# Optimization experiments

Measured on AMD Instinct MI355X. Metric: run time of the kernel, lower is better.

## Reference

```python
import jax, jax.numpy as jnp
import numpy as np

HIDDEN = 1024
HEADS = 16
B, L = 2, 2048


def _xavier(key, shape):
    fan_in, fan_out = shape[1], shape[0]
    limit = float(np.sqrt(6.0 / (fan_in + fan_out)))
    return jax.random.uniform(key, shape, jnp.float32, -limit, limit)


def setup_inputs() -> dict:
    key = jax.random.key(0)
    ks = jax.random.split(key, 6)
    return {
        "query": jax.random.normal(ks[0], (B, L, HIDDEN), jnp.float32),
        "bias": jax.random.normal(ks[1], (B, 1, 1, L), jnp.float32),
        "Wq": _xavier(ks[2], (HIDDEN, HIDDEN)), "bq": jnp.zeros((HIDDEN,), jnp.float32),
        "Wk": _xavier(ks[3], (HIDDEN, HIDDEN)), "bk": jnp.zeros((HIDDEN,), jnp.float32),
        "Wv": _xavier(ks[4], (HIDDEN, HIDDEN)), "bv": jnp.zeros((HIDDEN,), jnp.float32),
        "Wo": _xavier(ks[5], (HIDDEN, HIDDEN)), "bo": jnp.zeros((HIDDEN,), jnp.float32),
    }


def _split_heads(x):
    b, l, c = x.shape
    return x.reshape(b, l, HEADS, c // HEADS).transpose(0, 2, 1, 3)  # [B,H,L,d]


def reference(query, bias, Wq, bq, Wk, bk, Wv, bv, Wo, bo):
    d_head = HIDDEN // HEADS
    q = query @ Wq.T + bq
    k = query @ Wk.T + bk
    v = query @ Wv.T + bv
    q = _split_heads(q) * (d_head ** -0.5)  # [B,H,L,d]
    k = _split_heads(k)
    v = _split_heads(v)
    logits = jnp.einsum("bhqd,bhkd->bhqk", q, k) + bias  # [B,H,L,L]
    weights = jax.nn.softmax(logits, axis=-1)
    x = jnp.einsum("bhqk,bhkd->bhqd", weights, v)  # [B,H,L,d]
    x = x.transpose(0, 2, 1, 3).reshape(query.shape[0], query.shape[1], HIDDEN)
    return x @ Wo.T + bo
```

## Files before the change

### kernel.cpp

```cpp
#include <hip/hip_runtime.h>
#include <hip/hip_fp16.h>
#include <stdint.h>

#define HIDDEN 1024
#define HEADS  16
#define DH     64
#define B_     2
#define L_     2048
#define M_TOT  (B_ * L_)
#define ELEMS  (M_TOT * HIDDEN)
#define LOG2E  1.44269504088896340736f

typedef _Float16 f16;
typedef _Float16 f16x4 __attribute__((ext_vector_type(4)));
typedef _Float16 f16x8 __attribute__((ext_vector_type(8)));
typedef float    f32x4 __attribute__((ext_vector_type(4)));
typedef uint32_t u32;
typedef __attribute__((address_space(1))) u32 gu32;
typedef __attribute__((address_space(3))) u32 su32;

#define MFMA32(a, b, c) __builtin_amdgcn_mfma_f32_16x16x32_f16(a, b, c, 0, 0, 0)


__global__ __launch_bounds__(256)
void convert_f16(const float* __restrict__ query,
                 const float* __restrict__ Wq, const float* __restrict__ Wk,
                 const float* __restrict__ Wv, const float* __restrict__ Wo,
                 f16* __restrict__ Qh, f16* __restrict__ Wh)
{
    const int NQ4 = ELEMS / 4;
    const int NW4 = (HIDDEN * HIDDEN) / 4;
    const int total = NQ4 + 4 * NW4;
    for (int u = blockIdx.x * 256 + threadIdx.x; u < total; u += gridDim.x * 256) {
        float4 v; f16* dp;
        if (u < NQ4) {
            v = ((const float4*)query)[u];
            dp = Qh + (size_t)u * 4;
        } else {
            const int u2 = u - NQ4;
            const int w = u2 >> 18;
            const int off = u2 & (NW4 - 1);
            const float* W = (w == 0) ? Wq : (w == 1) ? Wk : (w == 2) ? Wv : Wo;
            v = ((const float4*)W)[off];
            dp = Wh + (size_t)u2 * 4;
        }
        f16x4 h = { (f16)v.x, (f16)v.y, (f16)v.z, (f16)v.w };
        *(f16x4*)dp = h;
    }
}

template<int TM, int TN, bool SWAP>
__device__ __forceinline__
void gemm_loop(const f16* __restrict__ A, const f16* __restrict__ W,
               int mb, int nb, f32x4 (&acc)[TM / 32][TN / 32])
{
    extern __shared__ f16 smem[];
    f16* As = smem;
    f16* Bs = smem + 3 * TM * 32;

    const int tid  = threadIdx.x;
    const int lane = tid & 63;
    const int wave = tid >> 6;
    const int quad = lane >> 4;
    const int l16  = lane & 15;
    const int wm   = (wave >> 1) * (TM / 2);
    const int wn   = (wave & 1) * (TN / 2);

    constexpr int AISS = TM / 64;
    constexpr int BISS = TN / 64;
    int aoff[AISS], boff[BISS];
#pragma unroll
    for (int q = 0; q < AISS; q++) {
        const int p16 = (wave * AISS + q) * 64 + lane;
        const int r = p16 >> 2;
        const int c8 = (p16 & 3) ^ ((r >> 1) & 3);
        aoff[q] = (mb + r) * HIDDEN + c8 * 8;
    }
#pragma unroll
    for (int q = 0; q < BISS; q++) {
        const int p16 = (wave * BISS + q) * 64 + lane;
        const int r = p16 >> 2;
        const int c8 = (p16 & 3) ^ ((r >> 1) & 3);
        boff[q] = (nb + r) * HIDDEN + c8 * 8;
    }

#pragma unroll
    for (int p = 0; p < 2; p++) {
#pragma unroll
        for (int q = 0; q < AISS; q++)
            __builtin_amdgcn_global_load_lds((gu32*)&A[aoff[q] + p * 32],
                                             (su32*)&As[p * TM * 32 + (wave * AISS + q) * 512], 16, 0, 0);
#pragma unroll
        for (int q = 0; q < BISS; q++)
            __builtin_amdgcn_global_load_lds((gu32*)&W[boff[q] + p * 32],
                                             (su32*)&Bs[p * TN * 32 + (wave * BISS + q) * 512], 16, 0, 0);
    }

    int sl = 0;
#pragma unroll 1
    for (int kb = 0; kb < HIDDEN; kb += 32) {
        if constexpr (AISS + BISS == 4)
            asm volatile("s_waitcnt vmcnt(4)" ::: "memory");
        else
            asm volatile("s_waitcnt vmcnt(3)" ::: "memory");
        __builtin_amdgcn_s_barrier();
        __builtin_amdgcn_sched_barrier(0);

        const int nkb = (kb + 64 < HIDDEN) ? kb + 64 : 0;
        const int si  = (sl >= 1) ? sl - 1 : 2;
#pragma unroll
        for (int q = 0; q < AISS; q++)
            __builtin_amdgcn_global_load_lds((gu32*)&A[aoff[q] + nkb],
                                             (su32*)&As[si * TM * 32 + (wave * AISS + q) * 512], 16, 0, 0);
#pragma unroll
        for (int q = 0; q < BISS; q++)
            __builtin_amdgcn_global_load_lds((gu32*)&W[boff[q] + nkb],
                                             (su32*)&Bs[si * TN * 32 + (wave * BISS + q) * 512], 16, 0, 0);

        f16x8 af[TM / 32], bf[TN / 32];
#pragma unroll
        for (int i = 0; i < TM / 32; i++) {
            const int r = wm + i * 16 + l16;
            af[i] = *(const f16x8*)&As[sl * TM * 32 + r * 32 + (quad ^ ((r >> 1) & 3)) * 8];
        }
#pragma unroll
        for (int j = 0; j < TN / 32; j++) {
            const int r = wn + j * 16 + l16;
            bf[j] = *(const f16x8*)&Bs[sl * TN * 32 + r * 32 + (quad ^ ((r >> 1) & 3)) * 8];
        }
#pragma unroll
        for (int i = 0; i < TM / 32; i++)
#pragma unroll
            for (int j = 0; j < TN / 32; j++) {
                if constexpr (SWAP)
                    acc[i][j] = MFMA32(bf[j], af[i], acc[i][j]);
                else
                    acc[i][j] = MFMA32(af[i], bf[j], acc[i][j]);
            }

        sl = (sl + 1 == 3) ? 0 : sl + 1;
    }
    asm volatile("s_waitcnt vmcnt(0)" ::: "memory");
}

__global__ __launch_bounds__(256)
void proj_qkv(const f16* __restrict__ A, const f16* __restrict__ W,
              const float* __restrict__ bq, const float* __restrict__ bk,
              const float* __restrict__ bv,
              f16* __restrict__ Qo, f16* __restrict__ Ko, f16* __restrict__ Vo)
{
    f32x4 acc[4][4] = {};
    const int mb = blockIdx.x * 128, nb = blockIdx.y * 128;
    const int nsel = nb >> 10;
    if (nsel < 2) gemm_loop<128, 128, true >(A, W, mb, nb, acc);
    else          gemm_loop<128, 128, false>(A, W, mb, nb, acc);

    const int lane = threadIdx.x & 63, wave = threadIdx.x >> 6;
    const int quad = lane >> 4, l16 = lane & 15;
    const int wm = (wave >> 1) * 64, wn = (wave & 1) * 64;
    const int nbase = nb & 1023;

    if (nsel < 2) {
        const float* bias = nsel ? bk : bq;
        f16* out = nsel ? Ko : Qo;
        const float scale = nsel ? 1.0f : 0.125f * LOG2E;
#pragma unroll
        for (int i = 0; i < 4; i++) {
            const int m = mb + wm + i * 16 + l16;
            const int b = m >> 11, l = m & (L_ - 1);
#pragma unroll
            for (int j = 0; j < 4; j++) {
                const int n0 = nbase + wn + j * 16 + quad * 4;
                const f32x4 bl4 = *(const f32x4*)&bias[n0];
                const int h = n0 >> 6, dd = n0 & 63;
                f16x4 pk;
#pragma unroll
                for (int r = 0; r < 4; r++)
                    pk[r] = (f16)((acc[i][j][r] + bl4[r]) * scale);
                *(f16x4*)&out[(((b * HEADS + h) * L_) + l) * DH + dd] = pk;
            }
        }
    } else {
#pragma unroll
        for (int i = 0; i < 4; i++)
#pragma unroll
            for (int j = 0; j < 4; j++) {
                const int n1 = nbase + wn + j * 16 + l16;
                const float bn = bv[n1];
                const int h = n1 >> 6, dd = n1 & 63;
                const int m0 = mb + wm + i * 16 + quad * 4;
                const int b = m0 >> 11, l0 = m0 & (L_ - 1);
                f16x4 pk;
#pragma unroll
                for (int r = 0; r < 4; r++) pk[r] = (f16)(acc[i][j][r] + bn);
                *(f16x4*)&Vo[((size_t)(b * HEADS + h) * DH + dd) * L_ + l0] = pk;
            }
    }
}

__global__ __launch_bounds__(256)
void proj_out(const f16* __restrict__ A, const f16* __restrict__ W,
              const float* __restrict__ bo, float* __restrict__ out)
{
    f32x4 acc[4][2] = {};
    const int mb = blockIdx.x * 128, nb = blockIdx.y * 64;
    gemm_loop<128, 64, true>(A, W, mb, nb, acc);

    const int lane = threadIdx.x & 63, wave = threadIdx.x >> 6;
    const int quad = lane >> 4, l16 = lane & 15;
    const int wm = (wave >> 1) * 64, wn = (wave & 1) * 32;
#pragma unroll
    for (int i = 0; i < 4; i++) {
        const int m = mb + wm + i * 16 + l16;
#pragma unroll
        for (int j = 0; j < 2; j++) {
            const int n0 = nb + wn + j * 16 + quad * 4;
            const float4 b4 = *(const float4*)&bo[n0];
            float4 st;
            st.x = acc[i][j][0] + b4.x;
            st.y = acc[i][j][1] + b4.y;
            st.z = acc[i][j][2] + b4.z;
            st.w = acc[i][j][3] + b4.w;
            *(float4*)&out[m * HIDDEN + n0] = st;
        }
    }
}

__global__ __launch_bounds__(512, 4)
void attn(const f16* __restrict__ Q, const f16* __restrict__ K,
          const f16* __restrict__ Vt, const float* __restrict__ bias,
          f16* __restrict__ X)
{
    __shared__ f16 Ks[2][2][64 * 64];
    __shared__ f16 Vs[2][2][64 * 64];
    __shared__ float biasl[L_];

    const int tid  = threadIdx.x;
    const int lane = tid & 63;
    const int wave = tid >> 6;
    const int quad = lane >> 4;
    const int l16  = lane & 15;
    const int qg   = wave >> 1;
    const int g    = wave & 1;

    const int bid = (int)blockIdx.x;
    const int lb  = (bid & 7) * 64 + (bid >> 3);
    const int bh  = lb >> 4;
    const int b   = bh >> 4, h = bh & 15;
    const int qrow0 = (lb & 15) * 128 + qg * 32;

    const f16* Qh  = Q  + (size_t)bh * L_ * DH;
    const f16* Kh  = K  + (size_t)bh * L_ * DH;
    const f16* Vth = Vt + (size_t)bh * DH * L_;

    {
        const float4 v = ((const float4*)(bias + b * L_))[tid];
        biasl[tid * 4 + 0] = v.x * LOG2E;
        biasl[tid * 4 + 1] = v.y * LOG2E;
        biasl[tid * 4 + 2] = v.z * LOG2E;
        biasl[tid * 4 + 3] = v.w * LOG2E;
    }

    int krow, kcol, vcol;
    {
        const int p = wave * 64 + lane;
        const int r = p >> 3;
        const int w8 = p & 7;
        krow = r;
        kcol = (w8 ^ (r & 7) ^ (((r >> 3) & 1) << 2)) * 8;
        vcol = (w8 ^ (r & 7)) * 8;
    }

    f16x8 qf[2][2];
#pragma unroll
    for (int qt = 0; qt < 2; qt++)
#pragma unroll
        for (int hh = 0; hh < 2; hh++)
            qf[qt][hh] = *(const f16x8*)&Qh[(qrow0 + qt * 16 + l16) * DH + hh * 32 + quad * 8];

    int koffX[2], koffY[2], voff[4];
    {
        const int rX = g * 32 + ((l16 >> 2) << 3) + (l16 & 3);
        const int rY = rX + 4;
        const int gkX = (rX & 7) ^ (((rX >> 3) & 1) << 2);
        const int gkY = (rY & 7) ^ (((rY >> 3) & 1) << 2);
#pragma unroll
        for (int hh = 0; hh < 2; hh++) {
            koffX[hh] = rX * 64 + (((hh * 4 + quad) ^ gkX) << 3);
            koffY[hh] = rY * 64 + (((hh * 4 + quad) ^ gkY) << 3);
        }
#pragma unroll
        for (int t = 0; t < 4; t++) {
            const int vr = t * 16 + l16;
            voff[t] = vr * 64 + (((g * 4 + quad) ^ (vr & 7)) << 3);
        }
    }

#pragma unroll
    for (int gi = 0; gi < 2; gi++) {
        __builtin_amdgcn_global_load_lds(
            (gu32*)(Kh + (size_t)(gi * 64 + krow) * DH + kcol),
            (su32*)&Ks[0][gi][wave * 512], 16, 0, 0);
        __builtin_amdgcn_global_load_lds(
            (gu32*)(Vth + (size_t)krow * L_ + gi * 64 + vcol),
            (su32*)&Vs[0][gi][wave * 512], 16, 0, 0);
    }

    f32x4 o[2][4] = {};
    f32x4 osum[2] = {};
    const f16x8 ones8 = { (f16)1.f, (f16)1.f, (f16)1.f, (f16)1.f,
                          (f16)1.f, (f16)1.f, (f16)1.f, (f16)1.f };
    __syncthreads();

#pragma unroll 1
    for (int kb = 0; kb < L_; kb += 128) {
        const int buf = (kb >> 7) & 1;
        const int nkb = (kb + 128 < L_) ? kb + 128 : 0;

#pragma unroll
        for (int gi = 0; gi < 2; gi++) {
            __builtin_amdgcn_global_load_lds(
                (gu32*)(Kh + (size_t)(nkb + gi * 64 + krow) * DH + kcol),
                (su32*)&Ks[buf ^ 1][gi][wave * 512], 16, 0, 0);
            __builtin_amdgcn_global_load_lds(
                (gu32*)(Vth + (size_t)krow * L_ + nkb + gi * 64 + vcol),
                (su32*)&Vs[buf ^ 1][gi][wave * 512], 16, 0, 0);
        }

#pragma unroll
        for (int gi = 0; gi < 2; gi++) {
            const f16* Kb = &Ks[buf][gi][0];
            const f16* Vb = &Vs[buf][gi][0];
            const f16x8 kx0 = *(const f16x8*)&Kb[koffX[0]];
            const f16x8 kx1 = *(const f16x8*)&Kb[koffX[1]];
            const f16x8 ky0 = *(const f16x8*)&Kb[koffY[0]];
            const f16x8 ky1 = *(const f16x8*)&Kb[koffY[1]];
            f16x8 va[4];
#pragma unroll
            for (int t = 0; t < 4; t++)
                va[t] = *(const f16x8*)&Vb[voff[t]];
            const f32x4 blvX = *(const f32x4*)&biasl[kb + gi * 64 + g * 32 + quad * 8];
            const f32x4 blvY = *(const f32x4*)&biasl[kb + gi * 64 + g * 32 + quad * 8 + 4];

#pragma unroll
            for (int qt = 0; qt < 2; qt++) {
                f32x4 zx = blvX, zy = blvY;
                zx = MFMA32(kx0, qf[qt][0], zx);
                zx = MFMA32(kx1, qf[qt][1], zx);
                zy = MFMA32(ky0, qf[qt][0], zy);
                zy = MFMA32(ky1, qf[qt][1], zy);
                const f16x8 pb = {
                    (f16)__builtin_amdgcn_exp2f(zx[0]), (f16)__builtin_amdgcn_exp2f(zx[1]),
                    (f16)__builtin_amdgcn_exp2f(zx[2]), (f16)__builtin_amdgcn_exp2f(zx[3]),
                    (f16)__builtin_amdgcn_exp2f(zy[0]), (f16)__builtin_amdgcn_exp2f(zy[1]),
                    (f16)__builtin_amdgcn_exp2f(zy[2]), (f16)__builtin_amdgcn_exp2f(zy[3]) };
#pragma unroll
                for (int t = 0; t < 4; t++)
                    o[qt][t] = MFMA32(va[t], pb, o[qt][t]);
                osum[qt] = MFMA32(ones8, pb, osum[qt]);
            }
        }
        __syncthreads();
    }

    float* o0 = (float*)Ks;
    float* o1 = (float*)Vs;
    if (g) {
#pragma unroll
        for (int t = 0; t < 4; t++)
#pragma unroll
            for (int r = 0; r < 4; r++) {
                o0[(qg * 16 + t * 4 + r) * 64 + lane] = o[0][t][r];
                o1[(qg * 16 + t * 4 + r) * 64 + lane] = o[1][t][r];
            }
        biasl[(qg * 64 + lane) * 2 + 0] = osum[0][0];
        biasl[(qg * 64 + lane) * 2 + 1] = osum[1][0];
    }
    __syncthreads();
    if (!g) {
#pragma unroll
        for (int t = 0; t < 4; t++)
#pragma unroll
            for (int r = 0; r < 4; r++) {
                o[0][t][r] += o0[(qg * 16 + t * 4 + r) * 64 + lane];
                o[1][t][r] += o1[(qg * 16 + t * 4 + r) * 64 + lane];
            }
        const float s0 = osum[0][0] + biasl[(qg * 64 + lane) * 2 + 0];
        const float s1 = osum[1][0] + biasl[(qg * 64 + lane) * 2 + 1];
#pragma unroll
        for (int qt = 0; qt < 2; qt++) {
            const float inv = 1.0f / (qt ? s1 : s0);
            const size_t qrow = (size_t)b * L_ + qrow0 + qt * 16 + l16;
#pragma unroll
            for (int t = 0; t < 4; t++) {
                f16x4 pk;
#pragma unroll
                for (int r = 0; r < 4; r++) pk[r] = (f16)(o[qt][t][r] * inv);
                *(f16x4*)&X[qrow * HIDDEN + h * DH + t * 16 + quad * 4] = pk;
            }
        }
    }
}

extern "C" void kernel_launch(void* const* d_in, const int* in_sizes, int n_in,
                              void* d_out, int out_size, void* d_ws, size_t ws_size,
                              hipStream_t stream)
{
    const float* query = (const float*)d_in[0];
    const float* bias  = (const float*)d_in[1];
    const float* Wq = (const float*)d_in[2]; const float* bq = (const float*)d_in[3];
    const float* Wk = (const float*)d_in[4]; const float* bk = (const float*)d_in[5];
    const float* Wv = (const float*)d_in[6]; const float* bv = (const float*)d_in[7];
    const float* Wo = (const float*)d_in[8]; const float* bo = (const float*)d_in[9];
    float* out = (float*)d_out;

    f16* Wh = (f16*)d_ws;
    f16* Qh = Wh + 4096 * 1024;
    f16* Kf = Qh + ELEMS;
    f16* Vf = Kf + ELEMS;
    f16* Qf = Vf + ELEMS;
    f16* Xf = Qh;

    convert_f16<<<2048, 256, 0, stream>>>(query, Wq, Wk, Wv, Wo, Qh, Wh);
    proj_qkv<<<dim3(32, 24), 256, 49152, stream>>>(Qh, Wh, bq, bk, bv, Qf, Kf, Vf);
    attn<<<512, 512, 0, stream>>>(Qf, Kf, Vf, bias, Xf);
    proj_out<<<dim3(32, 16), 256, 36864, stream>>>(Xf, Wh + 3072 * 1024, bo, out);
}
```

Before: 188.0 us.

## Split attention key chunks across twice as many waves with two-level reduction

The attention block grows from 512 to 1024 threads. Each wave now processes one 64-key sub-chunk per iteration instead of two, so four waves share each query group and each wave issues a single async K/V LDS load. Partial outputs and row sums are then combined in a two-stage LDS reduction. This raises wave-level parallelism and halves per-wave serial work, at the cost of extra barriers and reduction traffic, and it requires launch bounds of 1024 threads with 8 waves per EU.

```diff
diff --git a/kernel.cpp b/kernel.cpp
--- a/kernel.cpp
+++ b/kernel.cpp
@@ -226,7 +226,7 @@
     }
 }
 
-__global__ __launch_bounds__(512, 4)
+__global__ __launch_bounds__(1024, 8)
 void attn(const f16* __restrict__ Q, const f16* __restrict__ K,
           const f16* __restrict__ Vt, const float* __restrict__ bias,
           f16* __restrict__ X)
@@ -240,8 +240,12 @@
     const int wave = tid >> 6;
     const int quad = lane >> 4;
     const int l16  = lane & 15;
-    const int qg   = wave >> 1;
-    const int g    = wave & 1;
+    const int qg   = wave >> 2;
+    const int g4   = wave & 3;
+    const int cgi  = g4 >> 1;
+    const int g    = g4 & 1;
+    const int sgi  = wave >> 3;
+    const int sw   = wave & 7;
 
     const int bid = (int)blockIdx.x;
     const int lb  = (bid & 7) * 64 + (bid >> 3);
@@ -254,16 +258,14 @@
     const f16* Vth = Vt + (size_t)bh * DH * L_;
 
     {
-        const float4 v = ((const float4*)(bias + b * L_))[tid];
-        biasl[tid * 4 + 0] = v.x * LOG2E;
-        biasl[tid * 4 + 1] = v.y * LOG2E;
-        biasl[tid * 4 + 2] = v.z * LOG2E;
-        biasl[tid * 4 + 3] = v.w * LOG2E;
+        const float2 v2 = ((const float2*)(bias + b * L_))[tid];
+        biasl[tid * 2 + 0] = v2.x * LOG2E;
+        biasl[tid * 2 + 1] = v2.y * LOG2E;
     }
 
     int krow, kcol, vcol;
     {
-        const int p = wave * 64 + lane;
+        const int p = sw * 64 + lane;
         const int r = p >> 3;
         const int w8 = p & 7;
         krow = r;
@@ -296,15 +298,12 @@
         }
     }
 
-#pragma unroll
-    for (int gi = 0; gi < 2; gi++) {
-        __builtin_amdgcn_global_load_lds(
-            (gu32*)(Kh + (size_t)(gi * 64 + krow) * DH + kcol),
-            (su32*)&Ks[0][gi][wave * 512], 16, 0, 0);
-        __builtin_amdgcn_global_load_lds(
-            (gu32*)(Vth + (size_t)krow * L_ + gi * 64 + vcol),
-            (su32*)&Vs[0][gi][wave * 512], 16, 0, 0);
-    }
+    __builtin_amdgcn_global_load_lds(
+        (gu32*)(Kh + (size_t)(sgi * 64 + krow) * DH + kcol),
+        (su32*)&Ks[0][sgi][sw * 512], 16, 0, 0);
+    __builtin_amdgcn_global_load_lds(
+        (gu32*)(Vth + (size_t)krow * L_ + sgi * 64 + vcol),
+        (su32*)&Vs[0][sgi][sw * 512], 16, 0, 0);
 
     f32x4 o[2][4] = {};
     f32x4 osum[2] = {};
@@ -317,76 +316,97 @@
         const int buf = (kb >> 7) & 1;
         const int nkb = (kb + 128 < L_) ? kb + 128 : 0;
 
-#pragma unroll
-        for (int gi = 0; gi < 2; gi++) {
-            __builtin_amdgcn_global_load_lds(
-                (gu32*)(Kh + (size_t)(nkb + gi * 64 + krow) * DH + kcol),
-                (su32*)&Ks[buf ^ 1][gi][wave * 512], 16, 0, 0);
-            __builtin_amdgcn_global_load_lds(
-                (gu32*)(Vth + (size_t)krow * L_ + nkb + gi * 64 + vcol),
-                (su32*)&Vs[buf ^ 1][gi][wave * 512], 16, 0, 0);
-        }
-
-#pragma unroll
-        for (int gi = 0; gi < 2; gi++) {
-            const f16* Kb = &Ks[buf][gi][0];
-            const f16* Vb = &Vs[buf][gi][0];
-            const f16x8 kx0 = *(const f16x8*)&Kb[koffX[0]];
-            const f16x8 kx1 = *(const f16x8*)&Kb[koffX[1]];
-            const f16x8 ky0 = *(const f16x8*)&Kb[koffY[0]];
-            const f16x8 ky1 = *(const f16x8*)&Kb[koffY[1]];
-            f16x8 va[4];
+        __builtin_amdgcn_global_load_lds(
+            (gu32*)(Kh + (size_t)(nkb + sgi * 64 + krow) * DH + kcol),
+            (su32*)&Ks[buf ^ 1][sgi][sw * 512], 16, 0, 0);
+        __builtin_amdgcn_global_load_lds(
+            (gu32*)(Vth + (size_t)krow * L_ + nkb + sgi * 64 + vcol),
+            (su32*)&Vs[buf ^ 1][sgi][sw * 512], 16, 0, 0);
+
+        const f16* Kb = &Ks[buf][cgi][0];
+        const f16* Vb = &Vs[buf][cgi][0];
+        const f16x8 kx0 = *(const f16x8*)&Kb[koffX[0]];
+        const f16x8 kx1 = *(const f16x8*)&Kb[koffX[1]];
+        const f16x8 ky0 = *(const f16x8*)&Kb[koffY[0]];
+        const f16x8 ky1 = *(const f16x8*)&Kb[koffY[1]];
+        f16x8 va[4];
+#pragma unroll
+        for (int t = 0; t < 4; t++)
+            va[t] = *(const f16x8*)&Vb[voff[t]];
+        const f32x4 blvX = *(const f32x4*)&biasl[kb + cgi * 64 + g * 32 + quad * 8];
+        const f32x4 blvY = *(const f32x4*)&biasl[kb + cgi * 64 + g * 32 + quad * 8 + 4];
+
+#pragma unroll
+        for (int qt = 0; qt < 2; qt++) {
+            f32x4 zx = blvX, zy = blvY;
+            zx = MFMA32(kx0, qf[qt][0], zx);
+            zx = MFMA32(kx1, qf[qt][1], zx);
+            zy = MFMA32(ky0, qf[qt][0], zy);
+            zy = MFMA32(ky1, qf[qt][1], zy);
+            const f16x8 pb = {
+                (f16)__builtin_amdgcn_exp2f(zx[0]), (f16)__builtin_amdgcn_exp2f(zx[1]),
+                (f16)__builtin_amdgcn_exp2f(zx[2]), (f16)__builtin_amdgcn_exp2f(zx[3]),
+                (f16)__builtin_amdgcn_exp2f(zy[0]), (f16)__builtin_amdgcn_exp2f(zy[1]),
+                (f16)__builtin_amdgcn_exp2f(zy[2]), (f16)__builtin_amdgcn_exp2f(zy[3]) };
 #pragma unroll
             for (int t = 0; t < 4; t++)
-                va[t] = *(const f16x8*)&Vb[voff[t]];
-            const f32x4 blvX = *(const f32x4*)&biasl[kb + gi * 64 + g * 32 + quad * 8];
-            const f32x4 blvY = *(const f32x4*)&biasl[kb + gi * 64 + g * 32 + quad * 8 + 4];
-
-#pragma unroll
-            for (int qt = 0; qt < 2; qt++) {
-                f32x4 zx = blvX, zy = blvY;
-                zx = MFMA32(kx0, qf[qt][0], zx);
-                zx = MFMA32(kx1, qf[qt][1], zx);
-                zy = MFMA32(ky0, qf[qt][0], zy);
-                zy = MFMA32(ky1, qf[qt][1], zy);
-                const f16x8 pb = {
-                    (f16)__builtin_amdgcn_exp2f(zx[0]), (f16)__builtin_amdgcn_exp2f(zx[1]),
-                    (f16)__builtin_amdgcn_exp2f(zx[2]), (f16)__builtin_amdgcn_exp2f(zx[3]),
-                    (f16)__builtin_amdgcn_exp2f(zy[0]), (f16)__builtin_amdgcn_exp2f(zy[1]),
-                    (f16)__builtin_amdgcn_exp2f(zy[2]), (f16)__builtin_amdgcn_exp2f(zy[3]) };
-#pragma unroll
-                for (int t = 0; t < 4; t++)
-                    o[qt][t] = MFMA32(va[t], pb, o[qt][t]);
-                osum[qt] = MFMA32(ones8, pb, osum[qt]);
-            }
+                o[qt][t] = MFMA32(va[t], pb, o[qt][t]);
+            osum[qt] = MFMA32(ones8, pb, osum[qt]);
         }
         __syncthreads();
     }
 
-    float* o0 = (float*)Ks;
-    float* o1 = (float*)Vs;
-    if (g) {
+    float* r0 = (float*)Ks;
+    float* r1 = (float*)Vs;
+    float s0 = osum[0][0], s1 = osum[1][0];
+
+    const int s1slot = qg * 2 + cgi;
+    if (g4 & 1) {
 #pragma unroll
         for (int t = 0; t < 4; t++)
 #pragma unroll
             for (int r = 0; r < 4; r++) {
-                o0[(qg * 16 + t * 4 + r) * 64 + lane] = o[0][t][r];
-                o1[(qg * 16 + t * 4 + r) * 64 + lane] = o[1][t][r];
-            }
-        biasl[(qg * 64 + lane) * 2 + 0] = osum[0][0];
-        biasl[(qg * 64 + lane) * 2 + 1] = osum[1][0];
+                r0[s1slot * 1024 + (t * 4 + r) * 64 + lane] = o[0][t][r];
+                r1[s1slot * 1024 + (t * 4 + r) * 64 + lane] = o[1][t][r];
+            }
+        biasl[s1slot * 128 + lane * 2 + 0] = s0;
+        biasl[s1slot * 128 + lane * 2 + 1] = s1;
     }
     __syncthreads();
-    if (!g) {
+    if (!(g4 & 1)) {
 #pragma unroll
         for (int t = 0; t < 4; t++)
 #pragma unroll
             for (int r = 0; r < 4; r++) {
-                o[0][t][r] += o0[(qg * 16 + t * 4 + r) * 64 + lane];
-                o[1][t][r] += o1[(qg * 16 + t * 4 + r) * 64 + lane];
-            }
-        const float s0 = osum[0][0] + biasl[(qg * 64 + lane) * 2 + 0];
-        const float s1 = osum[1][0] + biasl[(qg * 64 + lane) * 2 + 1];
+                o[0][t][r] += r0[s1slot * 1024 + (t * 4 + r) * 64 + lane];
+                o[1][t][r] += r1[s1slot * 1024 + (t * 4 + r) * 64 + lane];
+            }
+        s0 += biasl[s1slot * 128 + lane * 2 + 0];
+        s1 += biasl[s1slot * 128 + lane * 2 + 1];
+    }
+    __syncthreads();
+    if (g4 == 2) {
+#pragma unroll
+        for (int t = 0; t < 4; t++)
+#pragma unroll
+            for (int r = 0; r < 4; r++) {
+                r0[qg * 1024 + (t * 4 + r) * 64 + lane] = o[0][t][r];
+                r1[qg * 1024 + (t * 4 + r) * 64 + lane] = o[1][t][r];
+            }
+        biasl[1024 + qg * 128 + lane * 2 + 0] = s0;
+        biasl[1024 + qg * 128 + lane * 2 + 1] = s1;
+    }
+    __syncthreads();
+    if (g4 == 0) {
+#pragma unroll
+        for (int t = 0; t < 4; t++)
+#pragma unroll
+            for (int r = 0; r < 4; r++) {
+                o[0][t][r] += r0[qg * 1024 + (t * 4 + r) * 64 + lane];
+                o[1][t][r] += r1[qg * 1024 + (t * 4 + r) * 64 + lane];
+            }
+        s0 += biasl[1024 + qg * 128 + lane * 2 + 0];
+        s1 += biasl[1024 + qg * 128 + lane * 2 + 1];
 #pragma unroll
         for (int qt = 0; qt < 2; qt++) {
             const float inv = 1.0f / (qt ? s1 : s0);
@@ -423,6 +443,6 @@
 
     convert_f16<<<2048, 256, 0, stream>>>(query, Wq, Wk, Wv, Wo, Qh, Wh);
     proj_qkv<<<dim3(32, 24), 256, 49152, stream>>>(Qh, Wh, bq, bk, bv, Qf, Kf, Vf);
-    attn<<<512, 512, 0, stream>>>(Qf, Kf, Vf, bias, Xf);
+    attn<<<512, 1024, 0, stream>>>(Qf, Kf, Vf, bias, Xf);
     proj_out<<<dim3(32, 16), 256, 36864, stream>>>(Xf, Wh + 3072 * 1024, bo, out);
 }
```

After: 553.9 us. 195% more time.

## Fuse fp32-to-fp16 conversion into projection GEMM loads, drop convert kernel

Applied to the files above, without the earlier changes.

Removes the separate conversion kernel and has the projection GEMMs read fp32 query and weights directly, converting to fp16 in registers before writing to LDS. The pipeline changes from a 3-stage async global_load_lds ring to a double-buffered register-staged scheme with __syncthreads each k-step. The intent is to save a kernel launch and the extra round trip of writing and re-reading fp16 copies. The cost is twice the global bytes per GEMM load, conversion ALU work inside the loop, and a shallower prefetch with heavier synchronisation.

```diff
diff --git a/kernel.cpp b/kernel.cpp
--- a/kernel.cpp
+++ b/kernel.cpp
@@ -22,41 +22,14 @@
 #define MFMA32(a, b, c) __builtin_amdgcn_mfma_f32_16x16x32_f16(a, b, c, 0, 0, 0)
 
 
-__global__ __launch_bounds__(256)
-void convert_f16(const float* __restrict__ query,
-                 const float* __restrict__ Wq, const float* __restrict__ Wk,
-                 const float* __restrict__ Wv, const float* __restrict__ Wo,
-                 f16* __restrict__ Qh, f16* __restrict__ Wh)
-{
-    const int NQ4 = ELEMS / 4;
-    const int NW4 = (HIDDEN * HIDDEN) / 4;
-    const int total = NQ4 + 4 * NW4;
-    for (int u = blockIdx.x * 256 + threadIdx.x; u < total; u += gridDim.x * 256) {
-        float4 v; f16* dp;
-        if (u < NQ4) {
-            v = ((const float4*)query)[u];
-            dp = Qh + (size_t)u * 4;
-        } else {
-            const int u2 = u - NQ4;
-            const int w = u2 >> 18;
-            const int off = u2 & (NW4 - 1);
-            const float* W = (w == 0) ? Wq : (w == 1) ? Wk : (w == 2) ? Wv : Wo;
-            v = ((const float4*)W)[off];
-            dp = Wh + (size_t)u2 * 4;
-        }
-        f16x4 h = { (f16)v.x, (f16)v.y, (f16)v.z, (f16)v.w };
-        *(f16x4*)dp = h;
-    }
-}
-
-template<int TM, int TN, bool SWAP>
+template<int TM, int TN, bool SWAP, bool A32, bool B32, typename TA, typename TB>
 __device__ __forceinline__
-void gemm_loop(const f16* __restrict__ A, const f16* __restrict__ W,
+void gemm_loop(const TA* __restrict__ A, const TB* __restrict__ W,
                int mb, int nb, f32x4 (&acc)[TM / 32][TN / 32])
 {
     extern __shared__ f16 smem[];
     f16* As = smem;
-    f16* Bs = smem + 3 * TM * 32;
+    f16* Bs = smem + 2 * TM * 32;
 
     const int tid  = threadIdx.x;
     const int lane = tid & 63;
@@ -68,13 +41,14 @@
 
     constexpr int AISS = TM / 64;
     constexpr int BISS = TN / 64;
-    int aoff[AISS], boff[BISS];
+    int aoff[AISS], boff[BISS], au[AISS], bu[BISS];
 #pragma unroll
     for (int q = 0; q < AISS; q++) {
         const int p16 = (wave * AISS + q) * 64 + lane;
         const int r = p16 >> 2;
         const int c8 = (p16 & 3) ^ ((r >> 1) & 3);
         aoff[q] = (mb + r) * HIDDEN + c8 * 8;
+        au[q] = p16;
     }
 #pragma unroll
     for (int q = 0; q < BISS; q++) {
@@ -82,51 +56,74 @@
         const int r = p16 >> 2;
         const int c8 = (p16 & 3) ^ ((r >> 1) & 3);
         boff[q] = (nb + r) * HIDDEN + c8 * 8;
-    }
-
-#pragma unroll
-    for (int p = 0; p < 2; p++) {
-#pragma unroll
-        for (int q = 0; q < AISS; q++)
-            __builtin_amdgcn_global_load_lds((gu32*)&A[aoff[q] + p * 32],
-                                             (su32*)&As[p * TM * 32 + (wave * AISS + q) * 512], 16, 0, 0);
-#pragma unroll
-        for (int q = 0; q < BISS; q++)
-            __builtin_amdgcn_global_load_lds((gu32*)&W[boff[q] + p * 32],
-                                             (su32*)&Bs[p * TN * 32 + (wave * BISS + q) * 512], 16, 0, 0);
-    }
-
-    int sl = 0;
+        bu[q] = p16;
+    }
+
+#pragma unroll
+    for (int q = 0; q < AISS; q++) {
+        if constexpr (A32) {
+            const float4 u0 = *(const float4*)&A[aoff[q]];
+            const float4 u1 = *(const float4*)&A[aoff[q] + 4];
+            f16x8 hv = { (f16)u0.x, (f16)u0.y, (f16)u0.z, (f16)u0.w,
+                         (f16)u1.x, (f16)u1.y, (f16)u1.z, (f16)u1.w };
+            *(f16x8*)&As[au[q] * 8] = hv;
+        } else {
+            __builtin_amdgcn_global_load_lds((gu32*)&A[aoff[q]],
+                                             (su32*)&As[(wave * AISS + q) * 512], 16, 0, 0);
+        }
+    }
+#pragma unroll
+    for (int q = 0; q < BISS; q++) {
+        if constexpr (B32) {
+            const float4 u0 = *(const float4*)&W[boff[q]];
+            const float4 u1 = *(const float4*)&W[boff[q] + 4];
+            f16x8 hv = { (f16)u0.x, (f16)u0.y, (f16)u0.z, (f16)u0.w,
+                         (f16)u1.x, (f16)u1.y, (f16)u1.z, (f16)u1.w };
+            *(f16x8*)&Bs[bu[q] * 8] = hv;
+        } else {
+            __builtin_amdgcn_global_load_lds((gu32*)&W[boff[q]],
+                                             (su32*)&Bs[(wave * BISS + q) * 512], 16, 0, 0);
+        }
+    }
+    __syncthreads();
+
 #pragma unroll 1
     for (int kb = 0; kb < HIDDEN; kb += 32) {
-        if constexpr (AISS + BISS == 4)
-            asm volatile("s_waitcnt vmcnt(4)" ::: "memory");
-        else
-            asm volatile("s_waitcnt vmcnt(3)" ::: "memory");
-        __builtin_amdgcn_s_barrier();
-        __builtin_amdgcn_sched_barrier(0);
-
-        const int nkb = (kb + 64 < HIDDEN) ? kb + 64 : 0;
-        const int si  = (sl >= 1) ? sl - 1 : 2;
-#pragma unroll
-        for (int q = 0; q < AISS; q++)
-            __builtin_amdgcn_global_load_lds((gu32*)&A[aoff[q] + nkb],
-                                             (su32*)&As[si * TM * 32 + (wave * AISS + q) * 512], 16, 0, 0);
-#pragma unroll
-        for (int q = 0; q < BISS; q++)
-            __builtin_amdgcn_global_load_lds((gu32*)&W[boff[q] + nkb],
-                                             (su32*)&Bs[si * TN * 32 + (wave * BISS + q) * 512], 16, 0, 0);
+        const int buf = (kb >> 5) & 1;
+        const int nkb = (kb + 32 < HIDDEN) ? kb + 32 : 0;
+
+        float4 fa0[AISS], fa1[AISS], fb0[BISS], fb1[BISS];
+#pragma unroll
+        for (int q = 0; q < AISS; q++) {
+            if constexpr (A32) {
+                fa0[q] = *(const float4*)&A[aoff[q] + nkb];
+                fa1[q] = *(const float4*)&A[aoff[q] + nkb + 4];
+            } else {
+                __builtin_amdgcn_global_load_lds((gu32*)&A[aoff[q] + nkb],
+                                                 (su32*)&As[(buf ^ 1) * TM * 32 + (wave * AISS + q) * 512], 16, 0, 0);
+            }
+        }
+#pragma unroll
+        for (int q = 0; q < BISS; q++) {
+            if constexpr (B32) {
+                fb0[q] = *(const float4*)&W[boff[q] + nkb];
+                fb1[q] = *(const float4*)&W[boff[q] + nkb + 4];
+            } else {
+                __builtin_amdgcn_global_load_lds((gu32*)&W[boff[q] + nkb],
+                                                 (su32*)&Bs[(buf ^ 1) * TN * 32 + (wave * BISS + q) * 512], 16, 0, 0);
+            }
+        }
 
         f16x8 af[TM / 32], bf[TN / 32];
 #pragma unroll
         for (int i = 0; i < TM / 32; i++) {
             const int r = wm + i * 16 + l16;
-            af[i] = *(const f16x8*)&As[sl * TM * 32 + r * 32 + (quad ^ ((r >> 1) & 3)) * 8];
+            af[i] = *(const f16x8*)&As[buf * TM * 32 + r * 32 + (quad ^ ((r >> 1) & 3)) * 8];
         }
 #pragma unroll
         for (int j = 0; j < TN / 32; j++) {
             const int r = wn + j * 16 + l16;
-            bf[j] = *(const f16x8*)&Bs[sl * TN * 32 + r * 32 + (quad ^ ((r >> 1) & 3)) * 8];
+            bf[j] = *(const f16x8*)&Bs[buf * TN * 32 + r * 32 + (quad ^ ((r >> 1) & 3)) * 8];
         }
 #pragma unroll
         for (int i = 0; i < TM / 32; i++)
@@ -138,27 +135,45 @@
                     acc[i][j] = MFMA32(af[i], bf[j], acc[i][j]);
             }
 
-        sl = (sl + 1 == 3) ? 0 : sl + 1;
-    }
-    asm volatile("s_waitcnt vmcnt(0)" ::: "memory");
+        if constexpr (A32) {
+#pragma unroll
+            for (int q = 0; q < AISS; q++) {
+                f16x8 hv = { (f16)fa0[q].x, (f16)fa0[q].y, (f16)fa0[q].z, (f16)fa0[q].w,
+                             (f16)fa1[q].x, (f16)fa1[q].y, (f16)fa1[q].z, (f16)fa1[q].w };
+                *(f16x8*)&As[(buf ^ 1) * TM * 32 + au[q] * 8] = hv;
+            }
+        }
+        if constexpr (B32) {
+#pragma unroll
+            for (int q = 0; q < BISS; q++) {
+                f16x8 hv = { (f16)fb0[q].x, (f16)fb0[q].y, (f16)fb0[q].z, (f16)fb0[q].w,
+                             (f16)fb1[q].x, (f16)fb1[q].y, (f16)fb1[q].z, (f16)fb1[q].w };
+                *(f16x8*)&Bs[(buf ^ 1) * TN * 32 + bu[q] * 8] = hv;
+            }
+        }
+        __syncthreads();
+    }
 }
 
 __global__ __launch_bounds__(256)
-void proj_qkv(const f16* __restrict__ A, const f16* __restrict__ W,
+void proj_qkv(const float* __restrict__ query,
+              const float* __restrict__ Wq, const float* __restrict__ Wk,
+              const float* __restrict__ Wv,
               const float* __restrict__ bq, const float* __restrict__ bk,
               const float* __restrict__ bv,
               f16* __restrict__ Qo, f16* __restrict__ Ko, f16* __restrict__ Vo)
 {
     f32x4 acc[4][4] = {};
-    const int mb = blockIdx.x * 128, nb = blockIdx.y * 128;
-    const int nsel = nb >> 10;
-    if (nsel < 2) gemm_loop<128, 128, true >(A, W, mb, nb, acc);
-    else          gemm_loop<128, 128, false>(A, W, mb, nb, acc);
+    const int mb = blockIdx.x * 128;
+    const int nsel  = blockIdx.y >> 3;
+    const int nbase = (blockIdx.y & 7) * 128;
+    const float* Wp = (nsel == 0) ? Wq : (nsel == 1) ? Wk : Wv;
+    if (nsel < 2) gemm_loop<128, 128, true , true, true>(query, Wp, mb, nbase, acc);
+    else          gemm_loop<128, 128, false, true, true>(query, Wp, mb, nbase, acc);
 
     const int lane = threadIdx.x & 63, wave = threadIdx.x >> 6;
     const int quad = lane >> 4, l16 = lane & 15;
     const int wm = (wave >> 1) * 64, wn = (wave & 1) * 64;
-    const int nbase = nb & 1023;
 
     if (nsel < 2) {
         const float* bias = nsel ? bk : bq;
@@ -199,12 +214,12 @@
 }
 
 __global__ __launch_bounds__(256)
-void proj_out(const f16* __restrict__ A, const f16* __restrict__ W,
+void proj_out(const f16* __restrict__ A, const float* __restrict__ Wo,
               const float* __restrict__ bo, float* __restrict__ out)
 {
     f32x4 acc[4][2] = {};
     const int mb = blockIdx.x * 128, nb = blockIdx.y * 64;
-    gemm_loop<128, 64, true>(A, W, mb, nb, acc);
+    gemm_loop<128, 64, true, false, true>(A, Wo, mb, nb, acc);
 
     const int lane = threadIdx.x & 63, wave = threadIdx.x >> 6;
     const int quad = lane >> 4, l16 = lane & 15;
@@ -414,15 +429,13 @@
     const float* Wo = (const float*)d_in[8]; const float* bo = (const float*)d_in[9];
     float* out = (float*)d_out;
 
-    f16* Wh = (f16*)d_ws;
-    f16* Qh = Wh + 4096 * 1024;
-    f16* Kf = Qh + ELEMS;
+    f16* Kf = (f16*)d_ws;
     f16* Vf = Kf + ELEMS;
     f16* Qf = Vf + ELEMS;
-    f16* Xf = Qh;
-
-    convert_f16<<<2048, 256, 0, stream>>>(query, Wq, Wk, Wv, Wo, Qh, Wh);
-    proj_qkv<<<dim3(32, 24), 256, 49152, stream>>>(Qh, Wh, bq, bk, bv, Qf, Kf, Vf);
+    f16* Xf = Qf + ELEMS;
+
+    proj_qkv<<<dim3(32, 24), 256, 32768, stream>>>(query, Wq, Wk, Wv,
+                                                   bq, bk, bv, Qf, Kf, Vf);
     attn<<<512, 512, 0, stream>>>(Qf, Kf, Vf, bias, Xf);
-    proj_out<<<dim3(32, 16), 256, 36864, stream>>>(Xf, Wh + 3072 * 1024, bo, out);
+    proj_out<<<dim3(32, 16), 256, 24576, stream>>>(Xf, Wo, bo, out);
 }
```

Result: slower. 210.2 us (+11.8%).
